# Kernel optimization log

Hardware: AMD Instinct MI355X
Metric: run time of the kernel (lower is better)

Reference implementation:

```python
import jax, jax.numpy as jnp
import numpy as np
from jax import lax

TAGSET_SIZE = 50
K = TAGSET_SIZE + 2          # +START, +STOP
START_TAG = TAGSET_SIZE      # 50
STOP_TAG = TAGSET_SIZE + 1   # 51
B, T = 1024, 512
NEG_INF = -10000.0


def setup_inputs() -> dict:
    key = jax.random.key(0)
    k1, k2, k3, k4 = jax.random.split(key, 4)
    logits = jax.random.normal(k1, (B, T, K), dtype=jnp.float32)
    transitions = jax.random.normal(k2, (K, K), dtype=jnp.float32)
    labels = jax.random.randint(k3, (B, T), 0, TAGSET_SIZE)          # real tags only
    lens = jax.random.randint(k4, (B,), 1, T + 1)                    # at least 1 token
    return {"logits": logits, "transitions": transitions, "labels": labels, "lens": lens}


def _crf_nll(logits, transitions, labels, lens):
    b, t, k = logits.shape

    # ---- forward algorithm (log partition) ----
    alpha0 = jnp.full((b, k), NEG_INF, dtype=logits.dtype).at[:, START_TAG].set(0.0)
    step_mask = jnp.arange(t)[None, :] < lens[:, None]               # [B,T] True while c_lens > 0

    def step(alpha, inp):
        logit_t, m_t = inp                                           # [B,K], [B]
        # alpha_nxt[b,i] = logsumexp_j(trans[i,j] + alpha[b,j]) + logit[b,i]
        mat = alpha[:, None, :] + transitions[None, :, :]            # [B,K,K]
        alpha_nxt = jax.nn.logsumexp(mat, axis=2) + logit_t
        alpha = jnp.where(m_t[:, None], alpha_nxt, alpha)
        return alpha, None

    alpha, _ = lax.scan(step, alpha0, (jnp.swapaxes(logits, 0, 1), step_mask.T))
    alpha = alpha + transitions[STOP_TAG][None, :]
    partition = jax.nn.logsumexp(alpha, axis=1)                      # [B]

    # ---- transition score of gold path ----
    start_col = jnp.full((b, 1), START_TAG, dtype=labels.dtype)
    stop_col = jnp.full((b, 1), STOP_TAG, dtype=labels.dtype)
    labels_ext = jnp.concatenate([start_col, labels, stop_col], axis=1)  # [B,T+2]
    pos = jnp.arange(t + 2)[None, :]
    keep = pos < (lens + 1)[:, None]                                 # positions <= lens keep tag, rest -> STOP
    labels_ext = jnp.where(keep, labels_ext, STOP_TAG)
    prev, nxt = labels_ext[:, :-1], labels_ext[:, 1:]                # [B,T+1]
    trn_scr = transitions[nxt, prev]                                 # trans[next, prev]
    m_trn = (jnp.arange(t + 1)[None, :] < (lens + 1)[:, None]).astype(logits.dtype)
    transition_score = jnp.sum(trn_scr * m_trn, axis=1)              # [B]

    # ---- emission score of gold path ----
    em = jnp.take_along_axis(logits, labels[:, :, None], axis=2)[:, :, 0]  # [B,T]
    m_em = (jnp.arange(t)[None, :] < lens[:, None]).astype(logits.dtype)
    emission_score = jnp.sum(em * m_em, axis=1)                      # [B]

    # faithful to source: partition + emission - transition
    return partition + emission_score - transition_score


def reference(logits, transitions, labels, lens):
    return _crf_nll(logits, transitions, labels, lens)
```

## Files before the change

### kernel.cpp

```cpp
#include <hip/hip_runtime.h>

#define KTAG 52
#define START_TAG 50
#define STOP_TAG 51
#define TMAX 512
#define NCU 256

__device__ __forceinline__ float rdlanef(float v, int l) {
    return __int_as_float(__builtin_amdgcn_readlane(__float_as_int(v), l));
}

__device__ __forceinline__ float matv(const float* __restrict__ Erow, float v) {
    float a0 = 0.f, a1 = 0.f, a2 = 0.f, a3 = 0.f;
    #pragma unroll
    for (int j = 0; j < 13; ++j) {
        a0 = fmaf(Erow[4*j+0], rdlanef(v, 4*j+0), a0);
        a1 = fmaf(Erow[4*j+1], rdlanef(v, 4*j+1), a1);
        a2 = fmaf(Erow[4*j+2], rdlanef(v, 4*j+2), a2);
        a3 = fmaf(Erow[4*j+3], rdlanef(v, 4*j+3), a3);
    }
    return (a0 + a1) + (a2 + a3);
}

template<bool BWD>
__device__ __forceinline__ float chain(const float* __restrict__ p0, int stride,
                                       int maxk, int nsteps, const float* __restrict__ Erow,
                                       float beta, float& M2) {
    constexpr float L2E = 1.4426950408889634f;
    M2 = 0.f;

    auto lgt = [&](int k) -> float {
        int kc = k < maxk ? k : maxk;
        return p0[(long)stride * kc];
    };
    auto STEP = [&](float lg, float scl) {
        float e = exp2f(lg * L2E);
        if (BWD) beta = matv(Erow, beta * e * scl);
        else     beta = matv(Erow, beta * scl) * e;
    };

    float l0 = lgt(0), l1 = lgt(1), l2 = lgt(2), l3 = lgt(3);
    int k = 0;
    while (k + 4 <= nsteps) {
        float n0 = lgt(k+4), n1 = lgt(k+5), n2 = lgt(k+6), n3 = lgt(k+7);
        float scl = 1.f;
        if (k > 0) {
            float m = fmaxf(rdlanef(beta, 0), 1e-30f);
            M2 += log2f(m);
            scl = 1.f / m;
        }
        STEP(l0, scl); STEP(l1, 1.f); STEP(l2, 1.f); STEP(l3, 1.f);
        l0 = n0; l1 = n1; l2 = n2; l3 = n3;
        k += 4;
    }
    if (k < nsteps) {
        float scl = 1.f;
        if (k > 0) {
            float m = fmaxf(rdlanef(beta, 0), 1e-30f);
            M2 += log2f(m);
            scl = 1.f / m;
        }
        STEP(l0, scl); ++k;
        if (k < nsteps) { STEP(l1, 1.f); ++k; }
        if (k < nsteps) { STEP(l2, 1.f); ++k; }
    }
    return beta;
}

#define LPL 16
__global__ __launch_bounds__(64) void rank_kernel(
    const int* __restrict__ lens, int* __restrict__ perm, int B)
{
    const int lane = threadIdx.x;
    int myl[LPL];
    #pragma unroll
    for (int k = 0; k < LPL; ++k) {
        int j = lane * LPL + k;
        myl[k] = (j < B) ? lens[j] : 0x7fffffff;
    }
    const int base = blockIdx.x * 64;
    for (int i = 0; i < 64; ++i) {
        int b = base + i;
        if (b >= B) break;
        int Lb = lens[b];
        int r = 0;
        #pragma unroll
        for (int k = 0; k < LPL; ++k) {
            int j = lane * LPL + k;
            r += (myl[k] < Lb || (myl[k] == Lb && j < b)) ? 1 : 0;
        }
        #pragma unroll
        for (int off = 32; off; off >>= 1) r += __shfl_xor(r, off);
        if (lane == 0) perm[r] = b;
    }
}

__global__ __launch_bounds__(128, 1) void crf_split_kernel(
    const float* __restrict__ logits,
    const float* __restrict__ trans,
    const int*   __restrict__ labels,
    const int*   __restrict__ lens,
    const int*   __restrict__ perm,
    float* __restrict__ out, int B)
{
    constexpr float L2E = 1.4426950408889634f;
    constexpr float LN2 = 0.6931471805599453f;

    const int blk  = blockIdx.x;
    const int wave = threadIdx.x >> 6;
    const int lane = threadIdx.x & 63;
    const bool active = lane < KTAG;
    const bool bwd = (wave == 1);

    int r = blk;
    if (B == 4 * NCU) {
        int m = blk & (NCU - 1), j = blk >> 8;
        r = (j == 0) ? m
          : (j == 1) ? (2 * NCU - 1 - m)
          : (j == 2) ? (2 * NCU + m)
          :            (4 * NCU - 1 - m);
    }
    const int batch = perm[r];
    const int len = lens[batch];
    const int mid = len >> 1;

    float Erow[KTAG];
    #pragma unroll
    for (int j = 0; j < KTAG; ++j) {
        float tv = active ? (bwd ? trans[j * KTAG + lane]
                                 : trans[(size_t)lane * KTAG + j]) : 0.f;
        Erow[j] = active ? exp2f(tv * L2E) : 0.f;
    }

    const float* base = logits + (size_t)batch * TMAX * KTAG + (active ? lane : 0);

    __shared__ __align__(16) float sB[64];
    __shared__ float sM2f, sEm, sTr;

    float M2, beta;
    if (bwd) {
        float b0 = active ? exp2f(trans[STOP_TAG * KTAG + lane] * L2E) : 0.f;
        beta = chain<true>(base + (size_t)(len - 1) * KTAG, -KTAG,
                           len - 1, len - mid, Erow, b0, M2);
    } else {
        float b0 = (lane == START_TAG) ? 1.f : 0.f;
        beta = chain<false>(base, KTAG, TMAX - 1, mid, Erow, b0, M2);

        const int*   labp = labels + (size_t)batch * TMAX;
        const float* lgb  = logits + (size_t)batch * TMAX * KTAG;
        int lab[8], prv[8]; bool msk[8];
        #pragma unroll
        for (int c = 0; c < 8; ++c) {
            int tt = c * 64 + lane;
            msk[c] = tt < len;
            int ttc = msk[c] ? tt : 0;
            lab[c] = labp[ttc];
            prv[c] = (ttc == 0) ? START_TAG : labp[ttc - 1];
        }
        float em = 0.f, tr = 0.f;
        #pragma unroll
        for (int c = 0; c < 8; ++c) {
            int ttc = msk[c] ? (c * 64 + lane) : 0;
            float ev = lgb[(size_t)ttc * KTAG + lab[c]];
            float tv = trans[lab[c] * KTAG + prv[c]];
            if (msk[c]) { em += ev; tr += tv; }
        }
        if (lane == 0) tr += trans[STOP_TAG * KTAG + labp[len - 1]];
        #pragma unroll
        for (int off = 32; off; off >>= 1) {
            em += __shfl_xor(em, off);
            tr += __shfl_xor(tr, off);
        }
        sB[lane] = beta;
        if (lane == 0) { sM2f = M2; sEm = em; sTr = tr; }
    }
    __syncthreads();

    if (bwd) {
        float d = beta * sB[lane];
        #pragma unroll
        for (int off = 32; off; off >>= 1) d += __shfl_xor(d, off);
        float partition = LN2 * (sM2f + M2 + log2f(d));
        if (lane == 0) out[batch] = partition + sEm - sTr;
    }
}

extern "C" void kernel_launch(void* const* d_in, const int* in_sizes, int n_in,
                              void* d_out, int out_size, void* d_ws, size_t ws_size,
                              hipStream_t stream) {
    const float* logits = (const float*)d_in[0];
    const float* trans  = (const float*)d_in[1];
    const int*   labels = (const int*)d_in[2];
    const int*   lens   = (const int*)d_in[3];
    float* out = (float*)d_out;

    const int B = in_sizes[3];
    int* perm = (int*)d_ws;

    rank_kernel<<<dim3((B + 63) / 64), dim3(64), 0, stream>>>(lens, perm, B);
    crf_split_kernel<<<dim3(B), dim3(128), 0, stream>>>(
        logits, trans, labels, lens, perm, out, B);
}
```

Before: 127.4 us.

## Broadcast beta via LDS float4 reads instead of 52 readlanes per step

Each recurrence step now writes the wave's beta vector to shared memory and reads it back as broadcast float4 loads, replacing 52 scalar readlane operations per matrix-vector product. The rank kernel takes the queried length from a register shuffle instead of a global load, and the block-to-rank mapping changes so that consecutive pairs of sorted lengths share a CU. This trades serialized SALU/readlane traffic for LDS latency on the critical dependency chain, and it relies on the in-wave write-then-read ordering without an explicit barrier.

```diff
diff --git a/kernel.cpp b/kernel.cpp
--- a/kernel.cpp
+++ b/kernel.cpp
@@ -10,21 +10,11 @@
     return __int_as_float(__builtin_amdgcn_readlane(__float_as_int(v), l));
 }
 
-__device__ __forceinline__ float matv(const float* __restrict__ Erow, float v) {
-    float a0 = 0.f, a1 = 0.f, a2 = 0.f, a3 = 0.f;
-    #pragma unroll
-    for (int j = 0; j < 13; ++j) {
-        a0 = fmaf(Erow[4*j+0], rdlanef(v, 4*j+0), a0);
-        a1 = fmaf(Erow[4*j+1], rdlanef(v, 4*j+1), a1);
-        a2 = fmaf(Erow[4*j+2], rdlanef(v, 4*j+2), a2);
-        a3 = fmaf(Erow[4*j+3], rdlanef(v, 4*j+3), a3);
-    }
-    return (a0 + a1) + (a2 + a3);
-}
-
 template<bool BWD>
 __device__ __forceinline__ float chain(const float* __restrict__ p0, int stride,
-                                       int maxk, int nsteps, const float* __restrict__ Erow,
+                                       int maxk, int nsteps,
+                                       const float* __restrict__ Erow,
+                                       float* sb, int lane,
                                        float beta, float& M2) {
     constexpr float L2E = 1.4426950408889634f;
     M2 = 0.f;
@@ -35,8 +25,20 @@
     };
     auto STEP = [&](float lg, float scl) {
         float e = exp2f(lg * L2E);
-        if (BWD) beta = matv(Erow, beta * e * scl);
-        else     beta = matv(Erow, beta * scl) * e;
+        float x = beta * scl;
+        if (BWD) x *= e;
+        sb[lane] = x;
+        float a0 = 0.f, a1 = 0.f, a2 = 0.f, a3 = 0.f;
+        #pragma unroll
+        for (int p = 0; p < 13; ++p) {
+            float4 bv = *reinterpret_cast<const float4*>(&sb[4 * p]);
+            a0 = fmaf(Erow[4*p+0], bv.x, a0);
+            a1 = fmaf(Erow[4*p+1], bv.y, a1);
+            a2 = fmaf(Erow[4*p+2], bv.z, a2);
+            a3 = fmaf(Erow[4*p+3], bv.w, a3);
+        }
+        float r = (a0 + a1) + (a2 + a3);
+        beta = BWD ? r : r * e;
     };
 
     float l0 = lgt(0), l1 = lgt(1), l2 = lgt(2), l3 = lgt(3);
@@ -79,10 +81,11 @@
         myl[k] = (j < B) ? lens[j] : 0x7fffffff;
     }
     const int base = blockIdx.x * 64;
+    const int Lme = (base + lane < B) ? lens[base + lane] : 0x7fffffff;
     for (int i = 0; i < 64; ++i) {
         int b = base + i;
         if (b >= B) break;
-        int Lb = lens[b];
+        int Lb = __shfl(Lme, i);
         int r = 0;
         #pragma unroll
         for (int k = 0; k < LPL; ++k) {
@@ -114,11 +117,11 @@
 
     int r = blk;
     if (B == 4 * NCU) {
-        int m = blk & (NCU - 1), j = blk >> 8;
-        r = (j == 0) ? m
-          : (j == 1) ? (2 * NCU - 1 - m)
-          : (j == 2) ? (2 * NCU + m)
-          :            (4 * NCU - 1 - m);
+        int q = blk & (NCU - 1), j = blk >> 8;
+        r = (j == 0) ? (2 * q)
+          : (j == 1) ? (2 * q + 1)
+          : (j == 2) ? (1022 - 2 * q)
+          :            (1023 - 2 * q);
     }
     const int batch = perm[r];
     const int len = lens[batch];
@@ -134,17 +137,18 @@
 
     const float* base = logits + (size_t)batch * TMAX * KTAG + (active ? lane : 0);
 
-    __shared__ __align__(16) float sB[64];
+    __shared__ __align__(16) float sbeta[2][64];
     __shared__ float sM2f, sEm, sTr;
 
     float M2, beta;
     if (bwd) {
         float b0 = active ? exp2f(trans[STOP_TAG * KTAG + lane] * L2E) : 0.f;
         beta = chain<true>(base + (size_t)(len - 1) * KTAG, -KTAG,
-                           len - 1, len - mid, Erow, b0, M2);
+                           len - 1, len - mid, Erow, &sbeta[1][0], lane, b0, M2);
     } else {
         float b0 = (lane == START_TAG) ? 1.f : 0.f;
-        beta = chain<false>(base, KTAG, TMAX - 1, mid, Erow, b0, M2);
+        beta = chain<false>(base, KTAG, TMAX - 1, mid, Erow,
+                            &sbeta[0][0], lane, b0, M2);
 
         const int*   labp = labels + (size_t)batch * TMAX;
         const float* lgb  = logits + (size_t)batch * TMAX * KTAG;
@@ -171,13 +175,13 @@
             em += __shfl_xor(em, off);
             tr += __shfl_xor(tr, off);
         }
-        sB[lane] = beta;
+        sbeta[0][lane] = beta;
         if (lane == 0) { sM2f = M2; sEm = em; sTr = tr; }
     }
     __syncthreads();
 
     if (bwd) {
-        float d = beta * sB[lane];
+        float d = beta * sbeta[0][lane];
         #pragma unroll
         for (int off = 32; off; off >>= 1) d += __shfl_xor(d, off);
         float partition = LN2 * (sM2f + M2 + log2f(d));
```

New measurement: 133.4 us. 4.7% more time.
